# Optimization experiments

Hardware: AMD Instinct MI355X
Metric: run time of the kernel (lower is better)

Reference implementation:

```python
import jax, jax.numpy as jnp
import numpy as np

N_HEADS = 16


def setup_inputs() -> dict:
    key = jax.random.key(0)
    ks = jax.random.split(key, 7)
    B, S, D = 2, 2048, 1024
    x = jax.random.normal(ks[0], (B, S, D), dtype=jnp.float32)
    attn_mask = jax.random.normal(ks[1], (S, S), dtype=jnp.float32) * 0.1
    attn_bias = jax.random.normal(ks[2], (B, S, S), dtype=jnp.float32) * 0.1
    Wqkv = jax.random.normal(ks[3], (D, 3 * D), dtype=jnp.float32) * (D ** -0.5)
    bqkv = jnp.zeros((3 * D,), dtype=jnp.float32)
    Wout = jax.random.normal(ks[4], (D, D), dtype=jnp.float32) * (D ** -0.5)
    bout = jnp.zeros((D,), dtype=jnp.float32)
    return {"x": x, "attn_mask": attn_mask, "attn_bias": attn_bias,
            "Wqkv": Wqkv, "bqkv": bqkv, "Wout": Wout, "bout": bout}


def reference(x, attn_mask, attn_bias, Wqkv, bqkv, Wout, bout):
    B, S, D = x.shape
    H = N_HEADS
    hd = D // H
    # qkv projection: [B,S,3D] -> [3,B,H,S,hd]
    qkv = (x @ Wqkv + bqkv).reshape(B, S, 3, H, hd).transpose(2, 0, 3, 1, 4)
    q, k, v = qkv[0], qkv[1], qkv[2]
    scores = jnp.einsum('bhqd,bhkd->bhqk', q, k) / (hd ** 0.5)
    scores = scores + attn_mask[None, None, :, :] + attn_bias[:, None, :, :]
    attn = jax.nn.softmax(scores, axis=-1)  # dropout p=0.0 (eval)
    out = jnp.einsum('bhqk,bhkd->bhqd', attn, v)
    out = out.transpose(0, 2, 1, 3).reshape(B, S, D)
    return out @ Wout + bout
```

## Files before the change

### kernel.cpp

```cpp
#include <hip/hip_runtime.h>
#include <hip/hip_bf16.h>


#define S_LEN 2048
#define DMODEL 1024
#define NH 16
#define HD 64

typedef __bf16 bf16x8 __attribute__((ext_vector_type(8)));
typedef __bf16 bf16x4 __attribute__((ext_vector_type(4)));
typedef __bf16 bf16x2v __attribute__((ext_vector_type(2)));
typedef float f32x4 __attribute__((ext_vector_type(4)));
typedef short s16x4 __attribute__((ext_vector_type(4)));

#define GLD_LDS16(g, l)                                              \
  __builtin_amdgcn_global_load_lds(                                  \
      (const __attribute__((address_space(1))) unsigned int*)(g),    \
      (__attribute__((address_space(3))) unsigned int*)(l), 16, 0, 0)

#if __has_builtin(__builtin_amdgcn_mfma_f32_16x16x16bf16_1k)
#define HAVE_MFMA_16x16x16_BF16 1
#else
#define HAVE_MFMA_16x16x16_BF16 0
#endif

#if __has_builtin(__builtin_amdgcn_exp2f)
#define EXP2F(x) __builtin_amdgcn_exp2f(x)
#else
static __device__ __forceinline__ float EXP2F(float x) {
  float r;
  asm volatile("v_exp_f32 %0, %1" : "=v"(r) : "v"(x));
  return r;
}
#endif

#define LOG2E 1.44269504f

__global__ __launch_bounds__(256) void preprocess(
    const float* __restrict__ x, const float* __restrict__ mask,
    const float* __restrict__ bias, const float* __restrict__ Wqkv,
    const float* __restrict__ Wout, __bf16* __restrict__ Xb,
    __bf16* __restrict__ Wt, __bf16* __restrict__ Wt2,
    __bf16* __restrict__ MB) {
  __shared__ __align__(16) char smem[64 * 65 * 4];
  const int bid = blockIdx.x;
  const int tid = threadIdx.x;

  if (bid < 4096) {
    int i = bid * 256 + tid;
    float4 v = ((const float4*)x)[i];
    bf16x4 o = {(__bf16)v.x, (__bf16)v.y, (__bf16)v.z, (__bf16)v.w};
    *(bf16x4*)&Xb[(size_t)i * 4] = o;
  } else if (bid < 5120) {
    const float* W;
    __bf16* Wo;
    int ncols, n0, k0;
    if (bid < 4864) {
      int id = bid - 4096;
      W = Wqkv; Wo = Wt; ncols = 3072;
      n0 = (id % 48) * 64; k0 = (id / 48) * 64;
    } else {
      int id = bid - 4864;
      W = Wout; Wo = Wt2; ncols = 1024;
      n0 = (id & 15) * 64; k0 = (id >> 4) * 64;
    }
    float(*tile)[65] = (float(*)[65])smem;
    {
      int c = tid & 63, r4 = tid >> 6;
#pragma unroll
      for (int p = 0; p < 16; ++p) {
        int r = r4 + p * 4;
        tile[r][c] = W[(size_t)(k0 + r) * ncols + n0 + c];
      }
    }
    __syncthreads();
    {
      int cc = (tid & 31) * 2, r8 = tid >> 5;
#pragma unroll
      for (int p = 0; p < 8; ++p) {
        int rr = r8 + p * 8;
        bf16x2v o = {(__bf16)tile[cc][rr], (__bf16)tile[cc + 1][rr]};
        *(bf16x2v*)&Wo[(size_t)(n0 + rr) * 1024 + k0 + cc] = o;
      }
    }
  } else {
    int id = bid - 5120;
    const int kt = id & 31, qt = id >> 5;
    __bf16(*sm)[68] = (__bf16(*)[68])smem;
    const int r0 = tid >> 4;
    const int cc = (tid & 15) * 4;
    const float* mrow = mask + (size_t)(qt * 64) * S_LEN + kt * 64;
    float4 mld[4];
#pragma unroll
    for (int p = 0; p < 4; ++p)
      mld[p] = *(const float4*)(mrow + (size_t)(r0 + p * 16) * S_LEN + cc);
    const int w = tid >> 6, lane = tid & 63;
    const int quad = lane >> 4, cl = lane & 15;
    for (int b = 0; b < 2; ++b) {
      const float* brow =
          bias + ((size_t)b * S_LEN + qt * 64) * S_LEN + kt * 64;
#pragma unroll
      for (int p = 0; p < 4; ++p) {
        int r = r0 + p * 16;
        float4 a = *(const float4*)(brow + (size_t)r * S_LEN + cc);
        sm[r][cc + 0] = (__bf16)((mld[p].x + a.x) * LOG2E);
        sm[r][cc + 1] = (__bf16)((mld[p].y + a.y) * LOG2E);
        sm[r][cc + 2] = (__bf16)((mld[p].z + a.z) * LOG2E);
        sm[r][cc + 3] = (__bf16)((mld[p].w + a.w) * LOG2E);
      }
      __syncthreads();
      __bf16 vals[16];
#pragma unroll
      for (int ct = 0; ct < 4; ++ct) {
        bf16x4 v = *(const bf16x4*)&sm[w * 16 + cl][ct * 16 + quad * 4];
        *(bf16x4*)&vals[ct * 4] = v;
      }
      __bf16* op = MB + (((size_t)(b * 32 + qt) * 32 + kt) * 4096) +
                   (w * 64 + lane) * 16;
      *(bf16x8*)op = *(bf16x8*)&vals[0];
      *(bf16x8*)(op + 8) = *(bf16x8*)&vals[8];
      __syncthreads();
    }
  }
}

__global__ __launch_bounds__(256) void gemm_qkv_mfma(
    const __bf16* __restrict__ Xb, const __bf16* __restrict__ Wt,
    const float* __restrict__ bqkv, __bf16* __restrict__ Qb,
    __bf16* __restrict__ Kb, __bf16* __restrict__ Vtb) {
  __shared__ __align__(16) __bf16 shm[4 * 64 * 72];
  __bf16* As = shm;
  __bf16* Bs = shm + 8192;
  const int tid = threadIdx.x;
  const int w = tid >> 6, lane = tid & 63;
  const int c = lane & 15, quad = lane >> 4;
  const int wm = w >> 1, wn = w & 1;
  const int rowBase = blockIdx.y * 128;
  const int colBase = blockIdx.x * 128;

  f32x4 acc[4][4] = {};

  const __bf16* gA0 =
      Xb + (size_t)(rowBase + w * 32 + (lane >> 2)) * 1024 + (lane & 3) * 8;
  const __bf16* gB0 =
      Wt + (size_t)(colBase + w * 32 + (lane >> 2)) * 1024 + (lane & 3) * 8;
  const int lOff = (w * 32) * 32;

#pragma unroll
  for (int p = 0; p < 2; ++p) {
    GLD_LDS16(gA0 + (size_t)p * 16 * 1024, As + lOff + p * 16 * 32);
    GLD_LDS16(gB0 + (size_t)p * 16 * 1024, Bs + lOff + p * 16 * 32);
  }
  __syncthreads();

#pragma unroll 2
  for (int k0 = 0; k0 < 1024; k0 += 32) {
    const int cur = (k0 >> 5) & 1, nxt = cur ^ 1;
    if (k0 < 992) {
#pragma unroll
      for (int p = 0; p < 2; ++p) {
        GLD_LDS16(gA0 + (size_t)p * 16 * 1024 + k0 + 32,
                  As + nxt * 4096 + lOff + p * 16 * 32);
        GLD_LDS16(gB0 + (size_t)p * 16 * 1024 + k0 + 32,
                  Bs + nxt * 4096 + lOff + p * 16 * 32);
      }
    }

    bf16x8 af[4], bfr[4];
#pragma unroll
    for (int mt = 0; mt < 4; ++mt)
      af[mt] = *(const bf16x8*)&As[cur * 4096 +
                                   (wm * 64 + mt * 16 + c) * 32 + quad * 8];
#pragma unroll
    for (int nt = 0; nt < 4; ++nt)
      bfr[nt] = *(const bf16x8*)&Bs[cur * 4096 +
                                    (wn * 64 + nt * 16 + c) * 32 + quad * 8];
#pragma unroll
    for (int mt = 0; mt < 4; ++mt)
#pragma unroll
      for (int nt = 0; nt < 4; ++nt)
        acc[mt][nt] = __builtin_amdgcn_mfma_f32_16x16x32_bf16(
            af[mt], bfr[nt], acc[mt][nt], 0, 0, 0);

    __syncthreads();
  }

  if (colBase < 2048) {
#pragma unroll
    for (int mt = 0; mt < 4; ++mt) {
      int row0 = rowBase + wm * 64 + mt * 16 + quad * 4;
#pragma unroll
      for (int nt = 0; nt < 4; ++nt) {
        int col = colBase + wn * 64 + nt * 16 + c;
        float bias = bqkv[col];
        int three = col >> 10;
        int h = (col & 1023) >> 6;
        int d = col & 63;
#pragma unroll
        for (int r = 0; r < 4; ++r) {
          int rr = row0 + r;
          int bb = rr >> 11, s = rr & 2047;
          float val = acc[mt][nt][r] + bias;
          size_t ho = (size_t)(bb * NH + h);
          if (three == 0)
            Qb[(ho * S_LEN + s) * HD + d] = (__bf16)val;
          else
            Kb[(ho * S_LEN + s) * HD + d] = (__bf16)val;
        }
      }
    }
  } else {
    __bf16* Tt = shm + w * (64 * 72);
    const int cols0 = colBase + wn * 64;
    const int rows0 = rowBase + wm * 64;
    const int hq = (cols0 & 1023) >> 6;
    const int bb = rows0 >> 11;
    const int sBase = rows0 & 2047;
#pragma unroll
    for (int nt = 0; nt < 4; ++nt) {
      float bias = bqkv[cols0 + nt * 16 + c];
#pragma unroll
      for (int mt = 0; mt < 4; ++mt) {
        __bf16 t4[4];
#pragma unroll
        for (int r = 0; r < 4; ++r) t4[r] = (__bf16)(acc[mt][nt][r] + bias);
        *(bf16x4*)&Tt[(nt * 16 + c) * 72 + mt * 16 + quad * 4] =
            *(bf16x4*)t4;
      }
    }
    __syncthreads();
    const size_t vbase = ((size_t)(bb * NH + hq) * HD) * S_LEN;
    const int s0 = (lane & 7) * 8;
    const int dl0 = lane >> 3;
#pragma unroll
    for (int dt = 0; dt < 8; ++dt) {
      int dl = dt * 8 + dl0;
      bf16x8 v = *(const bf16x8*)&Tt[dl * 72 + s0];
      *(bf16x8*)&Vtb[vbase + (size_t)dl * S_LEN + sBase + s0] = v;
    }
  }
}

__global__ __launch_bounds__(256) void attn_mfma(
    const __bf16* __restrict__ Qb, const __bf16* __restrict__ Kb,
    const __bf16* __restrict__ Vtb, const __bf16* __restrict__ MB,
    __bf16* __restrict__ AOb) {
  const int qt = blockIdx.x, h = blockIdx.y, b = blockIdx.z;
  const int tid = threadIdx.x;
  const int w = tid >> 6;
  const int lane = tid & 63;
  const int c = lane & 15;
  const int quad = lane >> 4;

  __shared__ __align__(16) __bf16 Ks[2][2][64 * 64];
  __shared__ __align__(16) __bf16 Vs[2][2][64 * 64];
#if !HAVE_MFMA_16x16x16_BF16
  __shared__ __align__(16) __bf16 P2[4][16 * 72];
#endif

  const size_t headoff = (size_t)(b * NH + h) * S_LEN * HD;
  const __bf16* Qg = Qb + headoff + (size_t)(qt * 128) * HD;
  const __bf16* Kg = Kb + headoff;
  const __bf16* Vg = Vtb + headoff;
  const __bf16* MBq0 =
      MB + ((size_t)(b * 32 + qt * 2 + 0) * 32) * 4096 + (w * 64 + lane) * 16;
  const __bf16* MBq1 =
      MB + ((size_t)(b * 32 + qt * 2 + 1) * 32) * 4096 + (w * 64 + lane) * 16;

  const int f0 = tid >> 3, f1 = f0 + 32;
  const int j = tid & 7;
  const int sj0 = j ^ (f0 & 7);
  const int sj1 = j ^ (f1 & 7);
  const int lds0 = tid * 8;
  const int lds1 = (256 + tid) * 8;

  bf16x8 qa[2][2];
#pragma unroll
  for (int g = 0; g < 2; ++g) {
    qa[g][0] = *(const bf16x8*)(Qg + (g * 64 + w * 16 + c) * HD + quad * 8);
    qa[g][1] =
        *(const bf16x8*)(Qg + (g * 64 + w * 16 + c) * HD + quad * 8 + 32);
  }

  const int rs0 = (quad ^ (c & 7)) * 8;
  const int rs1 = ((quad + 4) ^ (c & 7)) * 8;

  f32x4 Oa[2][4] = {};
  f32x4 psum[2] = {};

  const float c1 = 0.125f * LOG2E;

  auto subtile = [&](const __bf16* KsS, const __bf16* VsS,
                     bf16x8(&rmb)[2][2]) {
    bf16x8 kf0[4], kf1[4];
#pragma unroll
    for (int ct = 0; ct < 4; ++ct) {
      kf0[ct] = *(const bf16x8*)&KsS[(ct * 16 + c) * 64 + rs0];
      kf1[ct] = *(const bf16x8*)&KsS[(ct * 16 + c) * 64 + rs1];
    }
    f32x4 sv[2][4];
    __builtin_amdgcn_s_setprio(1);
#pragma unroll
    for (int g = 0; g < 2; ++g)
#pragma unroll
      for (int ct = 0; ct < 4; ++ct) {
        f32x4 a = {};
        a = __builtin_amdgcn_mfma_f32_16x16x32_bf16(kf0[ct], qa[g][0], a, 0,
                                                    0, 0);
        a = __builtin_amdgcn_mfma_f32_16x16x32_bf16(kf1[ct], qa[g][1], a, 0,
                                                    0, 0);
        sv[g][ct] = a;
      }
    __builtin_amdgcn_s_setprio(0);

#if HAVE_MFMA_16x16x16_BF16
    s16x4 vf[4][4];
#pragma unroll
    for (int ft = 0; ft < 4; ++ft) {
      const int fr = ft * 16 + c;
#pragma unroll
      for (int ct = 0; ct < 4; ++ct) {
        const int chunk = ((ct * 2 + (quad >> 1)) ^ (fr & 7)) * 8 +
                          (quad & 1) * 4;
        vf[ft][ct] = *(const s16x4*)&VsS[fr * 64 + chunk];
      }
    }
#endif

    s16x4 pb[2][4];
#pragma unroll
    for (int g = 0; g < 2; ++g)
#pragma unroll
      for (int ct = 0; ct < 4; ++ct) {
        f32x4 pv;
#pragma unroll
        for (int r = 0; r < 4; ++r) {
          float mb = (ct < 2) ? (float)rmb[g][0][ct * 4 + r]
                              : (float)rmb[g][1][(ct - 2) * 4 + r];
          pv[r] = EXP2F(sv[g][ct][r] * c1 + mb);
        }
        psum[g] += pv;
        __bf16 t4[4];
#pragma unroll
        for (int r = 0; r < 4; ++r) t4[r] = (__bf16)pv[r];
        pb[g][ct] = *(s16x4*)t4;
      }

#if HAVE_MFMA_16x16x16_BF16
    __builtin_amdgcn_s_setprio(1);
#pragma unroll
    for (int g = 0; g < 2; ++g)
#pragma unroll
      for (int ft = 0; ft < 4; ++ft)
#pragma unroll
        for (int ct = 0; ct < 4; ++ct)
          Oa[g][ft] = __builtin_amdgcn_mfma_f32_16x16x16bf16_1k(
              vf[ft][ct], pb[g][ct], Oa[g][ft], 0, 0, 0);
    __builtin_amdgcn_s_setprio(0);
#else
#pragma unroll
    for (int g = 0; g < 2; ++g) {
#pragma unroll
      for (int ct = 0; ct < 4; ++ct)
        *(bf16x4*)&P2[w][c * 72 + ct * 16 + quad * 4] = *(bf16x4*)&pb[g][ct];
      bf16x8 pf0 = *(const bf16x8*)&P2[w][c * 72 + quad * 8];
      bf16x8 pf1 = *(const bf16x8*)&P2[w][c * 72 + 32 + quad * 8];
#pragma unroll
      for (int ft = 0; ft < 4; ++ft) {
        const int fr = ft * 16 + c;
        bf16x8 vv0 = *(const bf16x8*)&VsS[fr * 64 + rs0];
        bf16x8 vv1 = *(const bf16x8*)&VsS[fr * 64 + rs1];
        Oa[g][ft] = __builtin_amdgcn_mfma_f32_16x16x32_bf16(vv0, pf0,
                                                            Oa[g][ft], 0, 0, 0);
        Oa[g][ft] = __builtin_amdgcn_mfma_f32_16x16x32_bf16(vv1, pf1,
                                                            Oa[g][ft], 0, 0, 0);
      }
    }
#endif
  };

  GLD_LDS16(Kg + (size_t)f0 * HD + sj0 * 8, &Ks[0][0][lds0]);
  GLD_LDS16(Kg + (size_t)f1 * HD + sj1 * 8, &Ks[0][0][lds1]);
  GLD_LDS16(Kg + (size_t)(64 + f0) * HD + sj0 * 8, &Ks[0][1][lds0]);
  GLD_LDS16(Kg + (size_t)(64 + f1) * HD + sj1 * 8, &Ks[0][1][lds1]);
  GLD_LDS16(Vg + (size_t)f0 * S_LEN + sj0 * 8, &Vs[0][0][lds0]);
  GLD_LDS16(Vg + (size_t)f1 * S_LEN + sj1 * 8, &Vs[0][0][lds1]);
  GLD_LDS16(Vg + (size_t)f0 * S_LEN + 64 + sj0 * 8, &Vs[0][1][lds0]);
  GLD_LDS16(Vg + (size_t)f1 * S_LEN + 64 + sj1 * 8, &Vs[0][1][lds1]);

  const __bf16* kgp0 = Kg + (size_t)(128 + f0) * HD + sj0 * 8;
  const __bf16* kgp1 = Kg + (size_t)(128 + f1) * HD + sj1 * 8;
  const __bf16* vgp0 = Vg + (size_t)f0 * S_LEN + 128 + sj0 * 8;
  const __bf16* vgp1 = Vg + (size_t)f1 * S_LEN + 128 + sj1 * 8;

  bf16x8 rMBA[2][2], rMBB[2][2];
  rMBA[0][0] = *(const bf16x8*)MBq0;
  rMBA[0][1] = *(const bf16x8*)(MBq0 + 8);
  rMBA[1][0] = *(const bf16x8*)MBq1;
  rMBA[1][1] = *(const bf16x8*)(MBq1 + 8);
  rMBB[0][0] = *(const bf16x8*)(MBq0 + 4096);
  rMBB[0][1] = *(const bf16x8*)(MBq0 + 4096 + 8);
  rMBB[1][0] = *(const bf16x8*)(MBq1 + 4096);
  rMBB[1][1] = *(const bf16x8*)(MBq1 + 4096 + 8);

  __syncthreads();

#pragma unroll 2
  for (int t = 0; t < 16; ++t) {
    const int cur = t & 1, nxt = cur ^ 1;
    if (t < 15) {
      GLD_LDS16(kgp0, &Ks[nxt][0][lds0]);
      GLD_LDS16(kgp1, &Ks[nxt][0][lds1]);
      GLD_LDS16(kgp0 + 64 * HD, &Ks[nxt][1][lds0]);
      GLD_LDS16(kgp1 + 64 * HD, &Ks[nxt][1][lds1]);
      GLD_LDS16(vgp0, &Vs[nxt][0][lds0]);
      GLD_LDS16(vgp1, &Vs[nxt][0][lds1]);
      GLD_LDS16(vgp0 + 64, &Vs[nxt][1][lds0]);
      GLD_LDS16(vgp1 + 64, &Vs[nxt][1][lds1]);
    }
    kgp0 += 128 * HD;
    kgp1 += 128 * HD;
    vgp0 += 128;
    vgp1 += 128;

    subtile(&Ks[cur][0][0], &Vs[cur][0][0], rMBA);

    bf16x8 nMBA[2][2], nMBB[2][2];
    {
      const __bf16* m0 = MBq0 + (size_t)(2 * t + 2) * 4096;
      const __bf16* m1 = MBq1 + (size_t)(2 * t + 2) * 4096;
      nMBA[0][0] = *(const bf16x8*)m0;
      nMBA[0][1] = *(const bf16x8*)(m0 + 8);
      nMBA[1][0] = *(const bf16x8*)m1;
      nMBA[1][1] = *(const bf16x8*)(m1 + 8);
      nMBB[0][0] = *(const bf16x8*)(m0 + 4096);
      nMBB[0][1] = *(const bf16x8*)(m0 + 4096 + 8);
      nMBB[1][0] = *(const bf16x8*)(m1 + 4096);
      nMBB[1][1] = *(const bf16x8*)(m1 + 4096 + 8);
    }

    subtile(&Ks[cur][1][0], &Vs[cur][1][0], rMBB);

#pragma unroll
    for (int g = 0; g < 2; ++g) {
      rMBA[g][0] = nMBA[g][0];
      rMBA[g][1] = nMBA[g][1];
      rMBB[g][0] = nMBB[g][0];
      rMBB[g][1] = nMBB[g][1];
    }

    __syncthreads();
  }

#pragma unroll
  for (int g = 0; g < 2; ++g) {
    float lsum = psum[g][0] + psum[g][1] + psum[g][2] + psum[g][3];
    lsum += __shfl_xor(lsum, 16);
    lsum += __shfl_xor(lsum, 32);
    const float invl = 1.0f / lsum;
    __bf16* orow = AOb +
                   (size_t)(b * S_LEN + qt * 128 + g * 64 + w * 16 + c) *
                       DMODEL +
                   h * HD;
#pragma unroll
    for (int ft = 0; ft < 4; ++ft) {
      __bf16 t4[4];
#pragma unroll
      for (int r = 0; r < 4; ++r) t4[r] = (__bf16)(Oa[g][ft][r] * invl);
      *(bf16x4*)(orow + ft * 16 + quad * 4) = *(bf16x4*)t4;
    }
  }
}

__global__ __launch_bounds__(256) void gemm_out_mfma(
    const __bf16* __restrict__ AOb, const __bf16* __restrict__ Wt2,
    const float* __restrict__ bout, float* __restrict__ Out) {
  __shared__ __align__(16) __bf16 As[2][128 * 32];
  __shared__ __align__(16) __bf16 Bs[2][64 * 32];
  const int tid = threadIdx.x;
  const int w = tid >> 6, lane = tid & 63;
  const int c = lane & 15, quad = lane >> 4;
  const int rowBase = blockIdx.y * 128;
  const int colBase = blockIdx.x * 64;

  f32x4 acc[2][4] = {};

  const __bf16* gA0 =
      AOb + (size_t)(rowBase + w * 32 + (lane >> 2)) * 1024 + (lane & 3) * 8;
  const __bf16* gB0 =
      Wt2 + (size_t)(colBase + w * 16 + (lane >> 2)) * 1024 + (lane & 3) * 8;
  const int lA = (w * 32) * 32;
  const int lB = (w * 16) * 32;

#pragma unroll
  for (int p = 0; p < 2; ++p)
    GLD_LDS16(gA0 + (size_t)p * 16 * 1024, &As[0][lA + p * 16 * 32]);
  GLD_LDS16(gB0, &Bs[0][lB]);
  __syncthreads();

#pragma unroll 2
  for (int k0 = 0; k0 < 1024; k0 += 32) {
    const int cur = (k0 >> 5) & 1, nxt = cur ^ 1;
    if (k0 < 992) {
#pragma unroll
      for (int p = 0; p < 2; ++p)
        GLD_LDS16(gA0 + (size_t)p * 16 * 1024 + k0 + 32,
                  &As[nxt][lA + p * 16 * 32]);
      GLD_LDS16(gB0 + k0 + 32, &Bs[nxt][lB]);
    }

    bf16x8 af[2], bfr[4];
#pragma unroll
    for (int mt = 0; mt < 2; ++mt)
      af[mt] =
          *(const bf16x8*)&As[cur][(w * 32 + mt * 16 + c) * 32 + quad * 8];
#pragma unroll
    for (int nt = 0; nt < 4; ++nt)
      bfr[nt] = *(const bf16x8*)&Bs[cur][(nt * 16 + c) * 32 + quad * 8];
#pragma unroll
    for (int mt = 0; mt < 2; ++mt)
#pragma unroll
      for (int nt = 0; nt < 4; ++nt)
        acc[mt][nt] = __builtin_amdgcn_mfma_f32_16x16x32_bf16(
            af[mt], bfr[nt], acc[mt][nt], 0, 0, 0);

    __syncthreads();
  }

#pragma unroll
  for (int mt = 0; mt < 2; ++mt) {
    int row0 = rowBase + w * 32 + mt * 16 + quad * 4;
#pragma unroll
    for (int nt = 0; nt < 4; ++nt) {
      int col = colBase + nt * 16 + c;
      float bias = bout[col];
#pragma unroll
      for (int r = 0; r < 4; ++r)
        Out[(size_t)(row0 + r) * 1024 + col] = acc[mt][nt][r] + bias;
    }
  }
}

extern "C" void kernel_launch(void* const* d_in, const int* in_sizes, int n_in,
                              void* d_out, int out_size, void* d_ws,
                              size_t ws_size, hipStream_t stream) {
  const float* x = (const float*)d_in[0];
  const float* attn_mask = (const float*)d_in[1];
  const float* attn_bias = (const float*)d_in[2];
  const float* Wqkv = (const float*)d_in[3];
  const float* bqkv = (const float*)d_in[4];
  const float* Wout = (const float*)d_in[5];
  const float* bout = (const float*)d_in[6];
  float* out = (float*)d_out;

  __bf16* base = (__bf16*)d_ws;
  __bf16* Xb = base;
  __bf16* AOb = base;
  __bf16* Wt = base + 4194304;
  __bf16* Qb = base + 8388608;
  __bf16* Kb = base + 12582912;
  __bf16* Vtb = base + 16777216;
  __bf16* MB = base + 20971520;
  __bf16* Wt2 = base + 29360128;

  preprocess<<<6144, 256, 0, stream>>>(x, attn_mask, attn_bias, Wqkv, Wout,
                                       Xb, Wt, Wt2, MB);
  gemm_qkv_mfma<<<dim3(24, 32), 256, 0, stream>>>(Xb, Wt, bqkv, Qb, Kb, Vtb);
  attn_mfma<<<dim3(16, NH, 2), 256, 0, stream>>>(Qb, Kb, Vtb, MB, AOb);
  gemm_out_mfma<<<dim3(16, 32), 256, 0, stream>>>(AOb, Wt2, bout, out);
}
```

Baseline: 252.5 us.

## Swizzle block indices across XCDs and deepen K-step in output GEMM

```diff
diff --git a/kernel.cpp b/kernel.cpp
--- a/kernel.cpp
+++ b/kernel.cpp
@@ -135,8 +135,12 @@
   const int w = tid >> 6, lane = tid & 63;
   const int c = lane & 15, quad = lane >> 4;
   const int wm = w >> 1, wn = w & 1;
-  const int rowBase = blockIdx.y * 128;
-  const int colBase = blockIdx.x * 128;
+
+  const int bid = blockIdx.y * 24 + blockIdx.x;
+  const int swz = (bid & 7) * 96 + (bid >> 3);
+  const int bx = swz % 24, by = swz / 24;
+  const int rowBase = by * 128;
+  const int colBase = bx * 128;
 
   f32x4 acc[4][4] = {};
 
@@ -245,7 +249,11 @@
     const __bf16* __restrict__ Qb, const __bf16* __restrict__ Kb,
     const __bf16* __restrict__ Vtb, const __bf16* __restrict__ MB,
     __bf16* __restrict__ AOb) {
-  const int qt = blockIdx.x, h = blockIdx.y, b = blockIdx.z;
+  const int bid = (blockIdx.z * 16 + blockIdx.y) * 16 + blockIdx.x;
+  const int swz = (bid & 7) * 64 + (bid >> 3);
+  const int qt = swz & 15;
+  const int h = (swz >> 4) & 15;
+  const int b = swz >> 8;
   const int tid = threadIdx.x;
   const int w = tid >> 6;
   const int lane = tid & 63;
@@ -475,13 +483,17 @@
 __global__ __launch_bounds__(256) void gemm_out_mfma(
     const __bf16* __restrict__ AOb, const __bf16* __restrict__ Wt2,
     const float* __restrict__ bout, float* __restrict__ Out) {
-  __shared__ __align__(16) __bf16 As[2][128 * 32];
-  __shared__ __align__(16) __bf16 Bs[2][64 * 32];
+  __shared__ __align__(16) __bf16 As[2][2][128 * 32];
+  __shared__ __align__(16) __bf16 Bs[2][2][64 * 32];
   const int tid = threadIdx.x;
   const int w = tid >> 6, lane = tid & 63;
   const int c = lane & 15, quad = lane >> 4;
-  const int rowBase = blockIdx.y * 128;
-  const int colBase = blockIdx.x * 64;
+
+  const int bid = blockIdx.y * 16 + blockIdx.x;
+  const int swz = (bid & 7) * 64 + (bid >> 3);
+  const int bx = swz & 15, by = swz >> 4;
+  const int rowBase = by * 128;
+  const int colBase = bx * 64;
 
   f32x4 acc[2][4] = {};
 
@@ -493,36 +505,47 @@
   const int lB = (w * 16) * 32;
 
 #pragma unroll
-  for (int p = 0; p < 2; ++p)
-    GLD_LDS16(gA0 + (size_t)p * 16 * 1024, &As[0][lA + p * 16 * 32]);
-  GLD_LDS16(gB0, &Bs[0][lB]);
+  for (int s = 0; s < 2; ++s) {
+#pragma unroll
+    for (int p = 0; p < 2; ++p)
+      GLD_LDS16(gA0 + (size_t)p * 16 * 1024 + s * 32,
+                &As[0][s][lA + p * 16 * 32]);
+    GLD_LDS16(gB0 + s * 32, &Bs[0][s][lB]);
+  }
   __syncthreads();
 
 #pragma unroll 2
-  for (int k0 = 0; k0 < 1024; k0 += 32) {
-    const int cur = (k0 >> 5) & 1, nxt = cur ^ 1;
-    if (k0 < 992) {
-#pragma unroll
-      for (int p = 0; p < 2; ++p)
-        GLD_LDS16(gA0 + (size_t)p * 16 * 1024 + k0 + 32,
-                  &As[nxt][lA + p * 16 * 32]);
-      GLD_LDS16(gB0 + k0 + 32, &Bs[nxt][lB]);
-    }
-
-    bf16x8 af[2], bfr[4];
-#pragma unroll
-    for (int mt = 0; mt < 2; ++mt)
-      af[mt] =
-          *(const bf16x8*)&As[cur][(w * 32 + mt * 16 + c) * 32 + quad * 8];
-#pragma unroll
-    for (int nt = 0; nt < 4; ++nt)
-      bfr[nt] = *(const bf16x8*)&Bs[cur][(nt * 16 + c) * 32 + quad * 8];
-#pragma unroll
-    for (int mt = 0; mt < 2; ++mt)
+  for (int t = 0; t < 16; ++t) {
+    const int cur = t & 1, nxt = cur ^ 1;
+    const int k0 = t * 64;
+    if (t < 15) {
+#pragma unroll
+      for (int s = 0; s < 2; ++s) {
+#pragma unroll
+        for (int p = 0; p < 2; ++p)
+          GLD_LDS16(gA0 + (size_t)p * 16 * 1024 + k0 + 64 + s * 32,
+                    &As[nxt][s][lA + p * 16 * 32]);
+        GLD_LDS16(gB0 + k0 + 64 + s * 32, &Bs[nxt][s][lB]);
+      }
+    }
+
+#pragma unroll
+    for (int s = 0; s < 2; ++s) {
+      bf16x8 af[2], bfr[4];
+#pragma unroll
+      for (int mt = 0; mt < 2; ++mt)
+        af[mt] = *(const bf16x8*)&As[cur][s]
+                                    [(w * 32 + mt * 16 + c) * 32 + quad * 8];
 #pragma unroll
       for (int nt = 0; nt < 4; ++nt)
-        acc[mt][nt] = __builtin_amdgcn_mfma_f32_16x16x32_bf16(
-            af[mt], bfr[nt], acc[mt][nt], 0, 0, 0);
+        bfr[nt] = *(const bf16x8*)&Bs[cur][s][(nt * 16 + c) * 32 + quad * 8];
+#pragma unroll
+      for (int mt = 0; mt < 2; ++mt)
+#pragma unroll
+        for (int nt = 0; nt < 4; ++nt)
+          acc[mt][nt] = __builtin_amdgcn_mfma_f32_16x16x32_bf16(
+              af[mt], bfr[nt], acc[mt][nt], 0, 0, 0);
+    }
 
     __syncthreads();
   }
```

Result: no change. 250.8 us (-0.7%).
